# Performance work log

Hardware: AMD Instinct MI355X
Metric: run time of the kernel (lower is better)

## Reference

```python
import jax, jax.numpy as jnp
import numpy as np

N = 40000       # nodes
E = 512000      # edges (avg degree 16)
D = 128         # embed_dim
H = 128         # hidden_dim
R = 8           # num_relations
B = 8           # num_bases
C = 3           # output classes (hardcoded in conv7)


def _prelu(x, a):
    # torch.nn.PReLU(num_parameters=C): per-channel slope
    return jnp.where(x >= 0, x, a * x)


def _rgcn(x, src, dst, etype, bases, comp, root, bias):
    """PyG RGCNConv with basis decomposition, aggr='mean' (default).
    out[i] = sum_r mean_{e: dst=i, type=r} (W_r @ x[src_e]) + root @ x[i] + bias
    W_r = sum_b comp[r,b] * bases[b]. Aggregation is linear, so we aggregate
    source features per (node, relation) first, then apply W_r once per node.
    """
    n = x.shape[0]
    seg = dst * R + etype                      # composite (node, relation) id
    gx = x[src]                                # [E, in]  (big gather)
    agg = jax.ops.segment_sum(gx, seg, num_segments=n * R)              # [N*R, in]
    cnt = jax.ops.segment_sum(jnp.ones((src.shape[0],), x.dtype), seg,
                              num_segments=n * R)                        # [N*R]
    agg = agg / jnp.maximum(cnt, 1.0)[:, None]                           # mean per (node, rel)
    agg = agg.reshape(n, R, -1)                                          # [N, R, in]
    Wr = jnp.einsum('rb,bio->rio', comp, bases)                          # [R, in, out]
    return jnp.einsum('nri,rio->no', agg, Wr) + x @ root + bias


def setup_inputs() -> dict:
    key = jax.random.key(0)
    ks = jax.random.split(key, 20)
    num_x = jax.random.normal(ks[0], (N, 1), jnp.float32)
    x = jax.random.normal(ks[1], (N, D), jnp.float32)
    edge_index = jax.random.randint(ks[2], (2, E), 0, N, jnp.int32)
    edge_type = jax.random.randint(ks[3], (E,), 0, R, jnp.int32)
    # params
    lin_w = jax.random.normal(ks[4], (1, D), jnp.float32) * 0.1
    lin_b = jax.random.normal(ks[5], (D,), jnp.float32) * 0.1
    prelu_a = 0.25 + 0.01 * jax.random.normal(ks[6], (7, D), jnp.float32)
    s = 1.0 / np.sqrt(H)
    bases = jax.random.normal(ks[7], (6, B, H, H), jnp.float32) * s   # conv1..conv6 (in==out==H)
    comp = jax.random.normal(ks[8], (6, R, B), jnp.float32) * (1.0 / np.sqrt(B))
    root = jax.random.normal(ks[9], (6, H, H), jnp.float32) * s
    bias = jax.random.normal(ks[10], (6, H), jnp.float32) * 0.1
    bases7 = jax.random.normal(ks[11], (B, H, C), jnp.float32) * s
    comp7 = jax.random.normal(ks[12], (R, B), jnp.float32) * (1.0 / np.sqrt(B))
    root7 = jax.random.normal(ks[13], (H, C), jnp.float32) * s
    bias7 = jax.random.normal(ks[14], (C,), jnp.float32) * 0.1
    return dict(num_x=num_x, x=x, edge_index=edge_index, edge_type=edge_type,
                lin_w=lin_w, lin_b=lin_b, prelu_a=prelu_a,
                bases=bases, comp=comp, root=root, bias=bias,
                bases7=bases7, comp7=comp7, root7=root7, bias7=bias7)


def reference(num_x, x, edge_index, edge_type, lin_w, lin_b, prelu_a,
              bases, comp, root, bias, bases7, comp7, root7, bias7):
    src, dst = edge_index[0], edge_index[1]
    h = _prelu(num_x @ lin_w + lin_b, prelu_a[0])   # act_lin(num_lin(num_x))
    h = h + x
    for i in range(6):  # conv1..conv6 + PReLU (dropout is identity in eval)
        h = _rgcn(h, src, dst, edge_type, bases[i], comp[i], root[i], bias[i])
        h = _prelu(h, prelu_a[i + 1])
    h = _rgcn(h, src, dst, edge_type, bases7, comp7, root7, bias7)  # conv7 -> 3 classes
    return jax.nn.log_softmax(h, axis=1)
```

## Files before the change

kernel.cpp:

```cpp
#include <hip/hip_runtime.h>

typedef unsigned short ushortT;
typedef ushortT ushort8 __attribute__((ext_vector_type(8)));
typedef short bf16x8 __attribute__((ext_vector_type(8)));
typedef float f32x4 __attribute__((ext_vector_type(4)));
typedef unsigned int uint32;

#define NN 40000
#define NE 512000
#define DD 128
#define RR 8
#define NSEG (NN * RR)
#define KT 1152
#define NB_SCAN 1250
#define ECAP 320

__device__ __forceinline__ float bf2f(ushortT u) { return __uint_as_float(((unsigned)u) << 16); }
__device__ __forceinline__ ushortT f2bf(float f) {
  unsigned u = __float_as_uint(f);
  unsigned r = (u + 0x7fffu + ((u >> 16) & 1u)) >> 16;
  return (ushortT)r;
}

__global__ void count_kernel(const int* __restrict__ dst, const int* __restrict__ et,
                             int* __restrict__ cnt) {
  int e = blockIdx.x * 256 + threadIdx.x;
  if (e < NE) atomicAdd(&cnt[dst[e] * RR + et[e]], 1);
}

__global__ void scan1_kernel(const int* __restrict__ cnt, int* __restrict__ offs,
                             int* __restrict__ bsum) {
  __shared__ int s[256];
  int tid = threadIdx.x, gid = blockIdx.x * 256 + tid;
  int v = cnt[gid];
  s[tid] = v; __syncthreads();
  for (int o = 1; o < 256; o <<= 1) {
    int t = (tid >= o) ? s[tid - o] : 0;
    __syncthreads(); s[tid] += t; __syncthreads();
  }
  offs[gid] = s[tid] - v;
  if (tid == 255) bsum[blockIdx.x] = s[255];
}

__global__ void scan2_kernel(int* __restrict__ bsum) {
  __shared__ int s[256];
  __shared__ int carry, tot;
  int tid = threadIdx.x;
  if (tid == 0) carry = 0;
  __syncthreads();
  for (int base = 0; base < NB_SCAN; base += 256) {
    int i = base + tid;
    int v = (i < NB_SCAN) ? bsum[i] : 0;
    s[tid] = v; __syncthreads();
    for (int o = 1; o < 256; o <<= 1) {
      int t = (tid >= o) ? s[tid - o] : 0;
      __syncthreads(); s[tid] += t; __syncthreads();
    }
    if (i < NB_SCAN) bsum[i] = s[tid] - v + carry;
    if (tid == 255) tot = s[255];
    __syncthreads();
    if (tid == 0) carry += tot;
    __syncthreads();
  }
}

__global__ void scan3_kernel(int* __restrict__ offs, const int* __restrict__ bsum,
                             const int* __restrict__ cnt, int* __restrict__ cursor) {
  int gid = blockIdx.x * 256 + threadIdx.x;
  int v = offs[gid] + bsum[blockIdx.x];
  offs[gid] = v;
  cursor[gid] = v;
  if (gid == NSEG - 1) offs[NSEG] = v + cnt[gid];
}

__global__ void fill_kernel(const int* __restrict__ src, const int* __restrict__ dst,
                            const int* __restrict__ et, int* __restrict__ cursor,
                            int* __restrict__ srcs) {
  int e = blockIdx.x * 256 + threadIdx.x;
  if (e >= NE) return;
  int seg = dst[e] * RR + et[e];
  int slot = atomicAdd(&cursor[seg], 1);
  srcs[slot] = src[e];
}

__global__ void init_h_kernel(const float* __restrict__ num_x, const float* __restrict__ x,
                              const float* __restrict__ lin_w, const float* __restrict__ lin_b,
                              const float* __restrict__ a0, ushortT* __restrict__ h) {
  int idx = blockIdx.x * 256 + threadIdx.x;
  if (idx >= NN * DD) return;
  int n = idx >> 7, d = idx & 127;
  float v = fmaf(num_x[n], lin_w[d], lin_b[d]);
  v = v >= 0.f ? v : a0[d] * v;
  h[idx] = f2bf(v + x[idx]);
}

__global__ void build_w_kernel(const float* __restrict__ bases, const float* __restrict__ comp,
                               const float* __restrict__ root, ushortT* __restrict__ Wt6) {
  int idx = blockIdx.x * 256 + threadIdx.x;
  if (idx >= 6 * DD * KT) return;
  int layer = idx / (DD * KT);
  int rem = idx - layer * (DD * KT);
  int j = rem / KT, k = rem - j * KT;
  const float* B  = bases + (size_t)layer * 8 * DD * DD;
  const float* C  = comp + layer * RR * 8;
  const float* Rt = root + (size_t)layer * DD * DD;
  float s;
  if (k < RR * DD) {
    int r = k >> 7, i = k & 127;
    s = 0.f;
#pragma unroll
    for (int b = 0; b < 8; ++b) s += C[r * 8 + b] * B[(b * DD + i) * DD + j];
  } else {
    s = Rt[(k - RR * DD) * DD + j];
  }
  Wt6[idx] = f2bf(s);
}

__global__ __launch_bounds__(256)
void agg_kernel(const int* __restrict__ offs, const int* __restrict__ srcs,
                const ushortT* __restrict__ h, ushortT* __restrict__ Xagg) {
  __shared__ int s_offs[33];
  __shared__ int s_srcs[ECAP];
  int tid = threadIdx.x;
  int sb = blockIdx.x * 32;
  if (tid < 33) s_offs[tid] = offs[sb + tid];
  __syncthreads();
  int e_base = s_offs[0];
  int nE = s_offs[32] - e_base;
  for (int i = tid; i < nE && i < ECAP; i += 256) s_srcs[i] = srcs[e_base + i];
  __syncthreads();

  int g = tid >> 3;
  int l = tid & 7;
  int beg = s_offs[g], end = s_offs[g + 1];
  float a[16];
#pragma unroll
  for (int j = 0; j < 16; ++j) a[j] = 0.f;
  int e = beg;
  for (; e + 2 <= end; e += 2) {
    int i0 = e - e_base, i1 = i0 + 1;
    int s0 = (i0 < ECAP) ? s_srcs[i0] : srcs[e];
    int s1 = (i1 < ECAP) ? s_srcs[i1] : srcs[e + 1];
    const ushortT* p0 = &h[(size_t)s0 * DD + l * 16];
    const ushortT* p1 = &h[(size_t)s1 * DD + l * 16];
    ushort8 v00 = *(const ushort8*)p0;
    ushort8 v01 = *(const ushort8*)(p0 + 8);
    ushort8 v10 = *(const ushort8*)p1;
    ushort8 v11 = *(const ushort8*)(p1 + 8);
#pragma unroll
    for (int j = 0; j < 8; ++j) {
      a[j]     += bf2f(v00[j]) + bf2f(v10[j]);
      a[8 + j] += bf2f(v01[j]) + bf2f(v11[j]);
    }
  }
  if (e < end) {
    int i0 = e - e_base;
    int s0 = (i0 < ECAP) ? s_srcs[i0] : srcs[e];
    const ushortT* p0 = &h[(size_t)s0 * DD + l * 16];
    ushort8 v00 = *(const ushort8*)p0;
    ushort8 v01 = *(const ushort8*)(p0 + 8);
#pragma unroll
    for (int j = 0; j < 8; ++j) {
      a[j]     += bf2f(v00[j]);
      a[8 + j] += bf2f(v01[j]);
    }
  }
  float inv = (end > beg) ? 1.0f / (float)(end - beg) : 1.0f;
  ushort8 r0, r1;
#pragma unroll
  for (int j = 0; j < 8; ++j) {
    r0[j] = f2bf(a[j] * inv);
    r1[j] = f2bf(a[8 + j] * inv);
  }
  ushortT* op = &Xagg[(size_t)(sb + g) * DD + l * 16];
  *(ushort8*)op = r0;
  *(ushort8*)(op + 8) = r1;
}

__global__ __launch_bounds__(256)
void gemm_kernel(const ushortT* __restrict__ Xagg, const ushortT* __restrict__ h,
                 const ushortT* __restrict__ Wt, const float* __restrict__ bias,
                 const float* __restrict__ slope, ushortT* __restrict__ hout) {
  __shared__ ushortT As[2][64 * 64];
  __shared__ ushortT Bs[2][128 * 64];
  int tid = threadIdx.x, lane = tid & 63, wv = tid >> 6;
  int wr = wv >> 1, wc = wv & 1;
  int n0 = blockIdx.x * 64;
  int l8 = lane >> 3;
  int lp = lane & 7;
  f32x4 acc[2][4];
#pragma unroll
  for (int m = 0; m < 2; ++m)
#pragma unroll
    for (int n = 0; n < 4; ++n) acc[m][n] = (f32x4){0.f, 0.f, 0.f, 0.f};

  auto stage = [&](int buf, int t) {
    int kc = t * 64;
#pragma unroll
    for (int j = 0; j < 2; ++j) {
      int row = wv * 16 + j * 8 + l8;
      int p = lp ^ (row & 7);
      const ushortT* g;
      if (kc < RR * DD) g = Xagg + (size_t)(n0 + row) * 1024 + kc + p * 8;
      else              g = h + (size_t)(n0 + row) * DD + (kc - RR * DD) + p * 8;
      __builtin_amdgcn_global_load_lds(
          (const __attribute__((address_space(1))) void*)g,
          (__attribute__((address_space(3))) void*)&As[buf][(wv * 16 + j * 8) * 64], 16, 0, 0);
    }
#pragma unroll
    for (int j = 0; j < 4; ++j) {
      int col = wv * 32 + j * 8 + l8;
      int p = lp ^ (col & 7);
      const ushortT* g = Wt + (size_t)col * KT + kc + p * 8;
      __builtin_amdgcn_global_load_lds(
          (const __attribute__((address_space(1))) void*)g,
          (__attribute__((address_space(3))) void*)&Bs[buf][(wv * 32 + j * 8) * 64], 16, 0, 0);
    }
  };

  stage(0, 0);
  __syncthreads();
  for (int t = 0; t < 18; ++t) {
    int cur = t & 1;
    if (t + 1 < 18) stage(cur ^ 1, t + 1);
#pragma unroll
    for (int kk = 0; kk < 2; ++kk) {
      int ko2 = kk * 64 + (lane >> 4) * 16;
      bf16x8 a[2], b[4];
#pragma unroll
      for (int m = 0; m < 2; ++m) {
        int row = wr * 32 + m * 16 + (lane & 15);
        int off = ((row << 7) + ko2) ^ ((row & 7) << 4);
        a[m] = *(const bf16x8*)((const char*)As[cur] + off);
      }
#pragma unroll
      for (int n = 0; n < 4; ++n) {
        int col = wc * 64 + n * 16 + (lane & 15);
        int off = ((col << 7) + ko2) ^ ((col & 7) << 4);
        b[n] = *(const bf16x8*)((const char*)Bs[cur] + off);
      }
#pragma unroll
      for (int m = 0; m < 2; ++m)
#pragma unroll
        for (int n = 0; n < 4; ++n)
          acc[m][n] = __builtin_amdgcn_mfma_f32_16x16x32_bf16(a[m], b[n], acc[m][n], 0, 0, 0);
    }
    __syncthreads();
  }
#pragma unroll
  for (int m = 0; m < 2; ++m) {
    int row = n0 + wr * 32 + m * 16 + (lane >> 4) * 4;
#pragma unroll
    for (int n = 0; n < 4; ++n) {
      int col = wc * 64 + n * 16 + (lane & 15);
      float bcol = bias[col], scol = slope[col];
#pragma unroll
      for (int q = 0; q < 4; ++q) {
        float v = acc[m][n][q] + bcol;
        v = v >= 0.f ? v : scol * v;
        hout[(size_t)(row + q) * DD + col] = f2bf(v);
      }
    }
  }
}

__global__ void build_w7_kernel(const float* __restrict__ bases7, const float* __restrict__ comp7,
                                const float* __restrict__ root7, float* __restrict__ W7) {
  int idx = blockIdx.x * 256 + threadIdx.x;
  if (idx >= KT * 3) return;
  int row = idx / 3, c = idx - row * 3;
  if (row < RR * DD) {
    int r = row >> 7, i = row & 127;
    float s = 0.f;
#pragma unroll
    for (int b = 0; b < 8; ++b) s += comp7[r * 8 + b] * bases7[(b * DD + i) * 3 + c];
    W7[idx] = s;
  } else {
    W7[idx] = root7[(row - RR * DD) * 3 + c];
  }
}

__global__ void conv7_kernel(const ushortT* __restrict__ Xagg, const ushortT* __restrict__ h,
                             const float* __restrict__ W7, const float* __restrict__ bias7,
                             float* __restrict__ out) {
  int gw = (blockIdx.x * 256 + threadIdx.x) >> 6;
  if (gw >= NN) return;
  int lane = threadIdx.x & 63;
  float a0 = 0.f, a1 = 0.f, a2 = 0.f;
#pragma unroll
  for (int i = 0; i < 2; ++i) {
    int k0 = i * 512 + lane * 8;
    ushort8 v = *(const ushort8*)&Xagg[(size_t)gw * 1024 + k0];
#pragma unroll
    for (int j = 0; j < 8; ++j) {
      float xx = bf2f(v[j]);
      const float* w = &W7[(k0 + j) * 3];
      a0 = fmaf(xx, w[0], a0); a1 = fmaf(xx, w[1], a1); a2 = fmaf(xx, w[2], a2);
    }
  }
  {
    uint32 v = *(const uint32*)&h[(size_t)gw * DD + lane * 2];
    float x0 = __uint_as_float(v << 16), x1 = __uint_as_float(v & 0xffff0000u);
    int k0 = 1024 + lane * 2;
    const float* w0 = &W7[k0 * 3];
    const float* w1 = &W7[(k0 + 1) * 3];
    a0 = fmaf(x0, w0[0], a0); a1 = fmaf(x0, w0[1], a1); a2 = fmaf(x0, w0[2], a2);
    a0 = fmaf(x1, w1[0], a0); a1 = fmaf(x1, w1[1], a1); a2 = fmaf(x1, w1[2], a2);
  }
#pragma unroll
  for (int o = 32; o > 0; o >>= 1) {
    a0 += __shfl_down(a0, o);
    a1 += __shfl_down(a1, o);
    a2 += __shfl_down(a2, o);
  }
  if (lane == 0) {
    float l0 = a0 + bias7[0], l1 = a1 + bias7[1], l2 = a2 + bias7[2];
    float m = fmaxf(l0, fmaxf(l1, l2));
    float lse = m + logf(expf(l0 - m) + expf(l1 - m) + expf(l2 - m));
    out[gw * 3 + 0] = l0 - lse;
    out[gw * 3 + 1] = l1 - lse;
    out[gw * 3 + 2] = l2 - lse;
  }
}

extern "C" void kernel_launch(void* const* d_in, const int* in_sizes, int n_in,
                              void* d_out, int out_size, void* d_ws, size_t ws_size,
                              hipStream_t stream) {
  const float* num_x  = (const float*)d_in[0];
  const float* x      = (const float*)d_in[1];
  const int*   eidx   = (const int*)d_in[2];
  const int*   etype  = (const int*)d_in[3];
  const float* lin_w  = (const float*)d_in[4];
  const float* lin_b  = (const float*)d_in[5];
  const float* prelu  = (const float*)d_in[6];
  const float* bases  = (const float*)d_in[7];
  const float* comp   = (const float*)d_in[8];
  const float* root   = (const float*)d_in[9];
  const float* bias   = (const float*)d_in[10];
  const float* bases7 = (const float*)d_in[11];
  const float* comp7  = (const float*)d_in[12];
  const float* root7  = (const float*)d_in[13];
  const float* bias7  = (const float*)d_in[14];
  const int* srcv = eidx;
  const int* dstv = eidx + NE;
  float* out = (float*)d_out;

  char* p = (char*)d_ws;
  auto alloc = [&](size_t bytes) { char* q = p; p += (bytes + 255) & ~(size_t)255; return q; };
  int*     counts = (int*)alloc((size_t)NSEG * 4);
  int*     offs   = (int*)alloc((size_t)(NSEG + 1) * 4);
  int*     cursor = (int*)alloc((size_t)NSEG * 4);
  int*     bsum   = (int*)alloc((size_t)NB_SCAN * 4);
  int*     srcs   = (int*)alloc((size_t)NE * 4);
  ushortT* h0     = (ushortT*)alloc((size_t)NN * DD * 2);
  ushortT* h1     = (ushortT*)alloc((size_t)NN * DD * 2);
  ushortT* Xagg   = (ushortT*)alloc((size_t)NN * 1024 * 2);
  ushortT* Wt6    = (ushortT*)alloc((size_t)6 * DD * KT * 2);
  float*   W7     = (float*)alloc((size_t)KT * 3 * 4);
  if (ws_size < (size_t)(p - (char*)d_ws)) return;

  hipMemsetAsync(counts, 0, (size_t)NSEG * 4, stream);
  count_kernel<<<NE / 256, 256, 0, stream>>>(dstv, etype, counts);
  scan1_kernel<<<NB_SCAN, 256, 0, stream>>>(counts, offs, bsum);
  scan2_kernel<<<1, 256, 0, stream>>>(bsum);
  scan3_kernel<<<NB_SCAN, 256, 0, stream>>>(offs, bsum, counts, cursor);
  fill_kernel<<<NE / 256, 256, 0, stream>>>(srcv, dstv, etype, cursor, srcs);

  init_h_kernel<<<(NN * DD + 255) / 256, 256, 0, stream>>>(num_x, x, lin_w, lin_b, prelu, h0);
  build_w_kernel<<<(6 * DD * KT + 255) / 256, 256, 0, stream>>>(bases, comp, root, Wt6);
  build_w7_kernel<<<(KT * 3 + 255) / 256, 256, 0, stream>>>(bases7, comp7, root7, W7);

  ushortT* hin = h0;
  ushortT* hout = h1;
  for (int layer = 0; layer < 6; ++layer) {
    agg_kernel<<<NSEG / 32, 256, 0, stream>>>(offs, srcs, hin, Xagg);
    gemm_kernel<<<NN / 64, 256, 0, stream>>>(Xagg, hin, Wt6 + (size_t)layer * DD * KT,
                                             bias + layer * DD, prelu + (layer + 1) * DD, hout);
    ushortT* t = hin; hin = hout; hout = t;
  }
  agg_kernel<<<NSEG / 32, 256, 0, stream>>>(offs, srcs, hin, Xagg);
  conv7_kernel<<<NN / 4, 256, 0, stream>>>(Xagg, hin, W7, bias7, out);
}
```

Before: 469.9 us.

## Fuse final-layer aggregation into conv7 using per-edge relation and mean weights

The last layer's separate aggregation pass, which wrote the full 1024-wide per-relation aggregate buffer, is removed. conv7 now walks each node's incoming edges directly, scales each source row by a precomputed 1/count weight and applies the relation-specific 3-column weights. The fill kernel packs the relation id into the high bits of the source index and writes a per-edge weight array. This drops one agg pass and a large write/read of Xagg. The cost is serialized per-edge loop latency inside conv7 and the assumption that node ids fit in 16 bits.

```diff
diff --git a/kernel.cpp b/kernel.cpp
--- a/kernel.cpp
+++ b/kernel.cpp
@@ -74,13 +74,16 @@
 }
 
 __global__ void fill_kernel(const int* __restrict__ src, const int* __restrict__ dst,
-                            const int* __restrict__ et, int* __restrict__ cursor,
-                            int* __restrict__ srcs) {
+                            const int* __restrict__ et, const int* __restrict__ cnt,
+                            int* __restrict__ cursor, int* __restrict__ edata,
+                            float* __restrict__ wgt) {
   int e = blockIdx.x * 256 + threadIdx.x;
   if (e >= NE) return;
-  int seg = dst[e] * RR + et[e];
+  int r = et[e];
+  int seg = dst[e] * RR + r;
   int slot = atomicAdd(&cursor[seg], 1);
-  srcs[slot] = src[e];
+  edata[slot] = src[e] | (r << 16);
+  wgt[slot] = 1.0f / (float)cnt[seg];
 }
 
 __global__ void init_h_kernel(const float* __restrict__ num_x, const float* __restrict__ x,
@@ -117,7 +120,7 @@
 }
 
 __global__ __launch_bounds__(256)
-void agg_kernel(const int* __restrict__ offs, const int* __restrict__ srcs,
+void agg_kernel(const int* __restrict__ offs, const int* __restrict__ edata,
                 const ushortT* __restrict__ h, ushortT* __restrict__ Xagg) {
   __shared__ int s_offs[33];
   __shared__ int s_srcs[ECAP];
@@ -127,7 +130,7 @@
   __syncthreads();
   int e_base = s_offs[0];
   int nE = s_offs[32] - e_base;
-  for (int i = tid; i < nE && i < ECAP; i += 256) s_srcs[i] = srcs[e_base + i];
+  for (int i = tid; i < nE && i < ECAP; i += 256) s_srcs[i] = edata[e_base + i];
   __syncthreads();
 
   int g = tid >> 3;
@@ -139,8 +142,8 @@
   int e = beg;
   for (; e + 2 <= end; e += 2) {
     int i0 = e - e_base, i1 = i0 + 1;
-    int s0 = (i0 < ECAP) ? s_srcs[i0] : srcs[e];
-    int s1 = (i1 < ECAP) ? s_srcs[i1] : srcs[e + 1];
+    int s0 = ((i0 < ECAP) ? s_srcs[i0] : edata[e]) & 0xFFFF;
+    int s1 = ((i1 < ECAP) ? s_srcs[i1] : edata[e + 1]) & 0xFFFF;
     const ushortT* p0 = &h[(size_t)s0 * DD + l * 16];
     const ushortT* p1 = &h[(size_t)s1 * DD + l * 16];
     ushort8 v00 = *(const ushort8*)p0;
@@ -155,7 +158,7 @@
   }
   if (e < end) {
     int i0 = e - e_base;
-    int s0 = (i0 < ECAP) ? s_srcs[i0] : srcs[e];
+    int s0 = ((i0 < ECAP) ? s_srcs[i0] : edata[e]) & 0xFFFF;
     const ushortT* p0 = &h[(size_t)s0 * DD + l * 16];
     ushort8 v00 = *(const ushort8*)p0;
     ushort8 v01 = *(const ushort8*)(p0 + 8);
@@ -280,32 +283,34 @@
   }
 }
 
-__global__ void conv7_kernel(const ushortT* __restrict__ Xagg, const ushortT* __restrict__ h,
-                             const float* __restrict__ W7, const float* __restrict__ bias7,
-                             float* __restrict__ out) {
+__global__ __launch_bounds__(256)
+void conv7_kernel(const int* __restrict__ offs, const int* __restrict__ edata,
+                  const float* __restrict__ wgt, const ushortT* __restrict__ h,
+                  const float* __restrict__ W7, const float* __restrict__ bias7,
+                  float* __restrict__ out) {
   int gw = (blockIdx.x * 256 + threadIdx.x) >> 6;
   if (gw >= NN) return;
   int lane = threadIdx.x & 63;
+  int beg = offs[gw * 8], end = offs[gw * 8 + 8];
   float a0 = 0.f, a1 = 0.f, a2 = 0.f;
-#pragma unroll
-  for (int i = 0; i < 2; ++i) {
-    int k0 = i * 512 + lane * 8;
-    ushort8 v = *(const ushort8*)&Xagg[(size_t)gw * 1024 + k0];
-#pragma unroll
-    for (int j = 0; j < 8; ++j) {
-      float xx = bf2f(v[j]);
-      const float* w = &W7[(k0 + j) * 3];
-      a0 = fmaf(xx, w[0], a0); a1 = fmaf(xx, w[1], a1); a2 = fmaf(xx, w[2], a2);
-    }
+  for (int e = beg; e < end; ++e) {
+    int ed = edata[e];
+    float w = wgt[e];
+    int src = ed & 0xFFFF;
+    int r = ed >> 16;
+    uint32 v = *(const uint32*)&h[(size_t)src * DD + lane * 2];
+    float x0 = __uint_as_float(v << 16) * w;
+    float x1 = __uint_as_float(v & 0xffff0000u) * w;
+    const float* wp = &W7[((r << 7) + lane * 2) * 3];
+    a0 = fmaf(x0, wp[0], a0); a1 = fmaf(x0, wp[1], a1); a2 = fmaf(x0, wp[2], a2);
+    a0 = fmaf(x1, wp[3], a0); a1 = fmaf(x1, wp[4], a1); a2 = fmaf(x1, wp[5], a2);
   }
   {
     uint32 v = *(const uint32*)&h[(size_t)gw * DD + lane * 2];
     float x0 = __uint_as_float(v << 16), x1 = __uint_as_float(v & 0xffff0000u);
-    int k0 = 1024 + lane * 2;
-    const float* w0 = &W7[k0 * 3];
-    const float* w1 = &W7[(k0 + 1) * 3];
-    a0 = fmaf(x0, w0[0], a0); a1 = fmaf(x0, w0[1], a1); a2 = fmaf(x0, w0[2], a2);
-    a0 = fmaf(x1, w1[0], a0); a1 = fmaf(x1, w1[1], a1); a2 = fmaf(x1, w1[2], a2);
+    const float* wp = &W7[(1024 + lane * 2) * 3];
+    a0 = fmaf(x0, wp[0], a0); a1 = fmaf(x0, wp[1], a1); a2 = fmaf(x0, wp[2], a2);
+    a0 = fmaf(x1, wp[3], a0); a1 = fmaf(x1, wp[4], a1); a2 = fmaf(x1, wp[5], a2);
   }
 #pragma unroll
   for (int o = 32; o > 0; o >>= 1) {
@@ -351,7 +356,8 @@
   int*     offs   = (int*)alloc((size_t)(NSEG + 1) * 4);
   int*     cursor = (int*)alloc((size_t)NSEG * 4);
   int*     bsum   = (int*)alloc((size_t)NB_SCAN * 4);
-  int*     srcs   = (int*)alloc((size_t)NE * 4);
+  int*     edata  = (int*)alloc((size_t)NE * 4);
+  float*   wgt    = (float*)alloc((size_t)NE * 4);
   ushortT* h0     = (ushortT*)alloc((size_t)NN * DD * 2);
   ushortT* h1     = (ushortT*)alloc((size_t)NN * DD * 2);
   ushortT* Xagg   = (ushortT*)alloc((size_t)NN * 1024 * 2);
@@ -364,7 +370,7 @@
   scan1_kernel<<<NB_SCAN, 256, 0, stream>>>(counts, offs, bsum);
   scan2_kernel<<<1, 256, 0, stream>>>(bsum);
   scan3_kernel<<<NB_SCAN, 256, 0, stream>>>(offs, bsum, counts, cursor);
-  fill_kernel<<<NE / 256, 256, 0, stream>>>(srcv, dstv, etype, cursor, srcs);
+  fill_kernel<<<NE / 256, 256, 0, stream>>>(srcv, dstv, etype, counts, cursor, edata, wgt);
 
   init_h_kernel<<<(NN * DD + 255) / 256, 256, 0, stream>>>(num_x, x, lin_w, lin_b, prelu, h0);
   build_w_kernel<<<(6 * DD * KT + 255) / 256, 256, 0, stream>>>(bases, comp, root, Wt6);
@@ -373,11 +379,10 @@
   ushortT* hin = h0;
   ushortT* hout = h1;
   for (int layer = 0; layer < 6; ++layer) {
-    agg_kernel<<<NSEG / 32, 256, 0, stream>>>(offs, srcs, hin, Xagg);
+    agg_kernel<<<NSEG / 32, 256, 0, stream>>>(offs, edata, hin, Xagg);
     gemm_kernel<<<NN / 64, 256, 0, stream>>>(Xagg, hin, Wt6 + (size_t)layer * DD * KT,
                                              bias + layer * DD, prelu + (layer + 1) * DD, hout);
     ushortT* t = hin; hin = hout; hout = t;
   }
-  agg_kernel<<<NSEG / 32, 256, 0, stream>>>(offs, srcs, hin, Xagg);
-  conv7_kernel<<<NN / 4, 256, 0, stream>>>(Xagg, hin, W7, bias7, out);
-}
+  conv7_kernel<<<NN / 4, 256, 0, stream>>>(offs, edata, wgt, hin, W7, bias7, out);
+}
```

Result: no change. 478.5 us (+1.8%).
